# Kernel optimization log

Hardware: AMD Instinct MI355X
Metric: run time of the kernel (lower is better)

## Reference

```python
import jax, jax.numpy as jnp
import numpy as np

N_USER = 100000
N_ITEM = 50000
D = 64
NNZ_A = 2000000
NNZ_S = 1000000
N_TAIL = 10000
N_HEAD = 4000
K = 10
B = 4096
N_NEG = 4
CONV = 40.0
ILAYERS = 3
SLAYERS = 2


def setup_inputs() -> dict:
    key = jax.random.key(0)
    ks = jax.random.split(key, 18)
    return {
        'user_emb': 0.1 * jax.random.normal(ks[0], (N_USER, D), jnp.float32),
        'item_emb': 0.1 * jax.random.normal(ks[1], (N_ITEM, D), jnp.float32),
        'w0': 0.05 * jax.random.normal(ks[2], (256, D), jnp.float32),
        'b0': 0.05 * jax.random.normal(ks[3], (256,), jnp.float32),
        'w2': 0.05 * jax.random.normal(ks[4], (D, 256), jnp.float32),
        'b2': 0.05 * jax.random.normal(ks[5], (D,), jnp.float32),
        'a_vals': jax.random.uniform(ks[6], (NNZ_A,), jnp.float32) * 0.1,
        's_vals': jax.random.uniform(ks[7], (NNZ_S,), jnp.float32) * 0.1,
        'item_degree': jax.random.uniform(ks[8], (N_ITEM,), jnp.float32) * 100.0,
        'a_rows': jax.random.randint(ks[9], (NNZ_A,), 0, N_USER + N_ITEM, jnp.int32),
        'a_cols': jax.random.randint(ks[10], (NNZ_A,), 0, N_USER + N_ITEM, jnp.int32),
        's_rows': jax.random.randint(ks[11], (NNZ_S,), 0, N_USER, jnp.int32),
        's_cols': jax.random.randint(ks[12], (NNZ_S,), 0, N_USER, jnp.int32),
        'tail_idx': jax.random.randint(ks[13], (N_TAIL,), 0, N_ITEM, jnp.int32),
        'head_idx': jax.random.randint(ks[14], (N_HEAD,), 0, N_ITEM, jnp.int32),
        'batch_user': jax.random.randint(ks[15], (B,), 0, N_USER, jnp.int32),
        'batch_pos': jax.random.randint(ks[16], (B,), 0, N_ITEM, jnp.int32),
        'batch_neg': jax.random.randint(ks[17], (B, N_NEG), 0, N_ITEM, jnp.int32),
    }


def _spmm(vals, rows, cols, x, n):
    # sparse.mm(A, x) with A in COO form; duplicate indices sum (coalesce/CSR semantics)
    return jax.ops.segment_sum(vals[:, None] * x[cols], rows, num_segments=n)


def reference(user_emb, item_emb, w0, b0, w2, b2, a_vals, s_vals, item_degree,
              a_rows, a_cols, s_rows, s_cols, tail_idx, head_idx,
              batch_user, batch_pos, batch_neg):
    # ---- item_link_predict_v1 (training branch: plain linear, no ReLU) ----
    def enc(f):
        return (f @ w0.T + b0) @ w2.T + b2
    tail_e = enc(item_emb[tail_idx])          # [N_TAIL, D]
    top_e = enc(item_emb[head_idx])           # [N_HEAD, D]
    scores = tail_e @ top_e.T                 # [N_TAIL, N_HEAD]
    topv, topi = jax.lax.top_k(scores, K)     # [N_TAIL, K]
    s = jax.nn.sigmoid(topv)
    w = s / (jnp.sum(s, axis=1, keepdims=True) + 1.0)
    ig_rows = jnp.repeat(tail_idx, K)         # tail index repeated per topk
    ig_cols = head_idx[topi].reshape(-1)
    ig_vals = jax.lax.stop_gradient(w.reshape(-1))  # original detaches enhance_weight
    # ---- interaction-graph propagation (LightGCN-style, last layer kept) ----
    n_total = N_USER + N_ITEM
    all_emb = jnp.concatenate([user_emb, item_emb], axis=0)
    for _ in range(ILAYERS):
        all_emb = _spmm(a_vals, a_rows, a_cols, all_emb, n_total)
    users = all_emb[:N_USER]
    items = all_emb[N_USER:]
    # ---- social-graph propagation, mean over layer outputs ----
    u_acc = users
    u = users
    for _ in range(SLAYERS):
        u = _spmm(s_vals, s_rows, s_cols, u, N_USER)
        u_acc = u_acc + u
    users_final = u_acc / float(SLAYERS + 1)
    # ---- item-similarity-graph enhancement with degree-based reweighting ----
    item_enh = _spmm(ig_vals, ig_rows, ig_cols, items, N_ITEM)
    sum_weight = CONV / (CONV + jnp.exp(item_degree / CONV))  # [N_ITEM]
    items_final = items + sum_weight[:, None] * item_enh
    # ---- BPR-style softplus loss + L2 reg on initial embeddings ----
    ue = users_final[batch_user]              # [B, D]
    pe = items_final[batch_pos]               # [B, D]
    ne = items_final[batch_neg]               # [B, N_NEG, D]
    pos_scores = jnp.sum(ue * pe, axis=1)
    neg_scores = jnp.mean(jnp.sum(ue[:, None, :] * ne, axis=2), axis=1)
    loss = jnp.mean(jax.nn.softplus(neg_scores - pos_scores))
    u0 = user_emb[batch_user]
    p0 = item_emb[batch_pos]
    n0 = item_emb[batch_neg]
    reg = 0.5 * (jnp.sum(u0 ** 2) + jnp.sum(p0 ** 2) + jnp.sum(n0 ** 2)) / float(B)
    return (loss, reg)
```

## Files before the change

### kernel.cpp

```cpp
#include <hip/hip_runtime.h>
#include <hip/hip_bf16.h>
#include <hip/hip_fp8.h>

#define N_USERC 100000
#define N_ITEMC 50000
#define N_TOTALC 150000
#define DC 64
#define NNZ_AC 2000000
#define NNZ_SC 1000000
#define N_TAILC 10000
#define N_HEADC 4000
#define TOPKC 10
#define BATCHC 4096
#define N_NEGC 4
#define CONVF 40.0f
#define CHUNK_ROWS 5000

#define RPB 256
#define NB_A ((N_TOTALC + RPB - 1) / RPB)
#define NB_S ((N_USERC + RPB - 1) / RPB)
#define IPB 6144
#define PBLK_A ((NNZ_AC + IPB - 1) / IPB)
#define PBLK_S ((NNZ_SC + IPB - 1) / IPB)
#define SLAB 4096
#define FCAP 4096

#define LOSS_BLOCKS (BATCHC / 4)

__device__ __forceinline__ unsigned char F2Q(float f) {
    __hip_fp8_e4m3 q(f);
    return (unsigned char)q.__x;
}
__device__ __forceinline__ float Q2F(unsigned char b) {
    __hip_fp8_e4m3 q;
    q.__x = (__hip_fp8_storage_t)b;
    return (float)q;
}
__device__ __forceinline__ unsigned short F2H(float f) {
    __hip_bfloat16 b = __float2bfloat16(f);
    return *(unsigned short*)&b;
}

__global__ __launch_bounds__(256) void init_cursors(int* __restrict__ aCur, int* __restrict__ sCur) {
    int i = blockIdx.x * 256 + threadIdx.x;
    if (i < NB_A) aCur[i] = i * SLAB;
    if (i < NB_S) sCur[i] = i * SLAB;
}

__global__ __launch_bounds__(256) void partition_fused(
    const float* __restrict__ a_vals, const int* __restrict__ a_rows, const int* __restrict__ a_cols,
    const float* __restrict__ s_vals, const int* __restrict__ s_rows, const int* __restrict__ s_cols,
    int* __restrict__ aCur, int* __restrict__ sCur,
    int2* __restrict__ aPack, int2* __restrict__ sPack) {
    __shared__ int h[NB_A];
    __shared__ int cur[NB_A];
    int blk = blockIdx.x;
    const float* vals; const int* rows; const int* cols; int n; int nb; int* gcur; int2* pack; int base;
    if (blk < PBLK_A) { vals = a_vals; rows = a_rows; cols = a_cols; n = NNZ_AC; nb = NB_A; gcur = aCur; pack = aPack; base = blk * IPB; }
    else { vals = s_vals; rows = s_rows; cols = s_cols; n = NNZ_SC; nb = NB_S; gcur = sCur; pack = sPack; base = (blk - PBLK_A) * IPB; }
    int tid = threadIdx.x;
    for (int i = tid; i < nb; i += 256) h[i] = 0;
    __syncthreads();
    for (int k = 0; k < IPB; k += 256) {
        int idx = base + k + tid;
        if (idx < n) atomicAdd(&h[rows[idx] >> 8], 1);
    }
    __syncthreads();
    for (int i = tid; i < nb; i += 256) {
        int c = h[i];
        cur[i] = c ? atomicAdd(&gcur[i], c) : 0;
    }
    __syncthreads();
    for (int k = 0; k < IPB; k += 256) {
        int idx = base + k + tid;
        if (idx < n) {
            int r = rows[idx];
            int b = r >> 8;
            int pos = atomicAdd(&cur[b], 1);
            pack[pos] = make_int2(__float_as_int(vals[idx]), cols[idx] | ((r & 255) << 18));
        }
    }
}

__global__ __launch_bounds__(256) void csr_finalize(const int* __restrict__ aEnd, const int* __restrict__ sEnd,
                                                    const int2* __restrict__ aRaw, const int2* __restrict__ sRaw,
                                                    int2* __restrict__ aOut, int2* __restrict__ sOut,
                                                    int* __restrict__ aRs, int* __restrict__ aRe,
                                                    int* __restrict__ sRs, int* __restrict__ sRe) {
    __shared__ int2 ebuf[FCAP];
    __shared__ int cnt_[RPB];
    __shared__ int scn[RPB];
    __shared__ int cursor[RPB];
    int blk = blockIdx.x;
    const int* ends; const int2* raw; int2* outp; int* rs; int* re; int nrows; int b;
    if (blk < NB_A) { ends = aEnd; raw = aRaw; outp = aOut; rs = aRs; re = aRe; nrows = N_TOTALC; b = blk; }
    else { ends = sEnd; raw = sRaw; outp = sOut; rs = sRs; re = sRe; nrows = N_USERC; b = blk - NB_A; }
    int s = b * SLAB;
    int e = ends[b];
    int n = e - s;
    int tid = threadIdx.x;
    bool useLds = (n <= FCAP);
    cnt_[tid] = 0;
    __syncthreads();
    if (useLds) {
        for (int i = tid; i < n; i += 256) {
            int2 en = raw[s + i];
            ebuf[i] = en;
            atomicAdd(&cnt_[(en.y >> 18) & 255], 1);
        }
    } else {
        for (int i = tid; i < n; i += 256)
            atomicAdd(&cnt_[(raw[s + i].y >> 18) & 255], 1);
    }
    __syncthreads();
    scn[tid] = cnt_[tid];
    __syncthreads();
    for (int off = 1; off < RPB; off <<= 1) {
        int t = (tid >= off) ? scn[tid - off] : 0;
        __syncthreads();
        scn[tid] += t;
        __syncthreads();
    }
    {
        int inc = scn[tid];
        int ex = inc - cnt_[tid];
        cursor[tid] = ex;
        int row = (b << 8) + tid;
        if (row < nrows) { rs[row] = s + ex; re[row] = s + inc; }
    }
    __syncthreads();
    if (useLds) {
        for (int i = tid; i < n; i += 256) {
            int2 en = ebuf[i];
            int r = (en.y >> 18) & 255;
            int pos = atomicAdd(&cursor[r], 1);
            outp[s + pos] = make_int2(en.x, en.y & 0x3FFFF);
        }
    } else {
        for (int i = tid; i < n; i += 256) {
            int2 en = raw[s + i];
            int r = (en.y >> 18) & 255;
            int pos = atomicAdd(&cursor[r], 1);
            outp[s + pos] = make_int2(en.x, en.y & 0x3FFFF);
        }
    }
}

__global__ __launch_bounds__(256) void to_f8_concat(const float* __restrict__ xu, const float* __restrict__ xi,
                                                    unsigned char* __restrict__ out) {
    size_t i4 = (size_t)blockIdx.x * 256 + threadIdx.x;
    const size_t NU4 = (size_t)N_USERC * 16;
    const size_t NT4 = (size_t)N_TOTALC * 16;
    if (i4 >= NT4) return;
    float4 v = (i4 < NU4) ? ((const float4*)xu)[i4] : ((const float4*)xi)[i4 - NU4];
    uchar4 q;
    q.x = F2Q(v.x); q.y = F2Q(v.y); q.z = F2Q(v.z); q.w = F2Q(v.w);
    ((uchar4*)out)[i4] = q;
}

__global__ __launch_bounds__(256) void spmm_f8(const int* __restrict__ rps, const int* __restrict__ rpe,
                                               const int2* __restrict__ pack,
                                               const unsigned char* __restrict__ xq,
                                               float* __restrict__ y,
                                               unsigned char* __restrict__ yq, int nrows) {
    int w = (blockIdx.x * blockDim.x + threadIdx.x) >> 6;
    int lane = threadIdx.x & 63;
    if (w >= nrows) return;
    int half = lane >> 5;
    int sl = lane & 31;
    int s = rps[w], e = rpe[w];
    float a0 = 0.f, a1 = 0.f, b0 = 0.f, b1 = 0.f;
    float c0 = 0.f, c1 = 0.f, d0 = 0.f, d1 = 0.f;
    if (e > s) {
        int last = e - 1;
        for (int j = s; j < e; j += 16) {
            int k0 = j + half, k1 = k0 + 2, k2 = k0 + 4, k3 = k0 + 6;
            int k4 = k0 + 8, k5 = k0 + 10, k6 = k0 + 12, k7 = k0 + 14;
            int2 e0 = pack[min(k0, last)], e1 = pack[min(k1, last)];
            int2 e2 = pack[min(k2, last)], e3 = pack[min(k3, last)];
            int2 e4 = pack[min(k4, last)], e5 = pack[min(k5, last)];
            int2 e6 = pack[min(k6, last)], e7 = pack[min(k7, last)];
            unsigned short g0 = *(const unsigned short*)&xq[(size_t)e0.y * 64 + sl * 2];
            unsigned short g1 = *(const unsigned short*)&xq[(size_t)e1.y * 64 + sl * 2];
            unsigned short g2 = *(const unsigned short*)&xq[(size_t)e2.y * 64 + sl * 2];
            unsigned short g3 = *(const unsigned short*)&xq[(size_t)e3.y * 64 + sl * 2];
            unsigned short g4 = *(const unsigned short*)&xq[(size_t)e4.y * 64 + sl * 2];
            unsigned short g5 = *(const unsigned short*)&xq[(size_t)e5.y * 64 + sl * 2];
            unsigned short g6 = *(const unsigned short*)&xq[(size_t)e6.y * 64 + sl * 2];
            unsigned short g7 = *(const unsigned short*)&xq[(size_t)e7.y * 64 + sl * 2];
            float v0 = (k0 <= last) ? __int_as_float(e0.x) : 0.f;
            float v1 = (k1 <= last) ? __int_as_float(e1.x) : 0.f;
            float v2 = (k2 <= last) ? __int_as_float(e2.x) : 0.f;
            float v3 = (k3 <= last) ? __int_as_float(e3.x) : 0.f;
            float v4 = (k4 <= last) ? __int_as_float(e4.x) : 0.f;
            float v5 = (k5 <= last) ? __int_as_float(e5.x) : 0.f;
            float v6 = (k6 <= last) ? __int_as_float(e6.x) : 0.f;
            float v7 = (k7 <= last) ? __int_as_float(e7.x) : 0.f;
            a0 += v0 * Q2F((unsigned char)(g0 & 255)); a1 += v0 * Q2F((unsigned char)(g0 >> 8));
            b0 += v1 * Q2F((unsigned char)(g1 & 255)); b1 += v1 * Q2F((unsigned char)(g1 >> 8));
            c0 += v2 * Q2F((unsigned char)(g2 & 255)); c1 += v2 * Q2F((unsigned char)(g2 >> 8));
            d0 += v3 * Q2F((unsigned char)(g3 & 255)); d1 += v3 * Q2F((unsigned char)(g3 >> 8));
            a0 += v4 * Q2F((unsigned char)(g4 & 255)); a1 += v4 * Q2F((unsigned char)(g4 >> 8));
            b0 += v5 * Q2F((unsigned char)(g5 & 255)); b1 += v5 * Q2F((unsigned char)(g5 >> 8));
            c0 += v6 * Q2F((unsigned char)(g6 & 255)); c1 += v6 * Q2F((unsigned char)(g6 >> 8));
            d0 += v7 * Q2F((unsigned char)(g7 & 255)); d1 += v7 * Q2F((unsigned char)(g7 >> 8));
        }
    }
    float r0 = (a0 + b0) + (c0 + d0);
    float r1 = (a1 + b1) + (c1 + d1);
    r0 += __shfl_xor(r0, 32, 64);
    r1 += __shfl_xor(r1, 32, 64);
    if (lane < 32) {
        if (y) ((float2*)y)[(size_t)w * 32 + sl] = make_float2(r0, r1);
        if (yq) { uchar2 q; q.x = F2Q(r0); q.y = F2Q(r1); ((uchar2*)yq)[(size_t)w * 32 + sl] = q; }
    }
}

__global__ __launch_bounds__(256) void mc_kernel(const float* __restrict__ w0, const float* __restrict__ b0,
                                                 const float* __restrict__ w2, const float* __restrict__ b2,
                                                 float* __restrict__ Mrm, float* __restrict__ cvec) {
    int idx = blockIdx.x * 256 + threadIdx.x;
    if (idx < 4096) {
        int j = idx >> 6, d = idx & 63;
        float acc = 0.f;
        for (int k = 0; k < 256; ++k) acc += w2[j * 256 + k] * w0[k * 64 + d];
        Mrm[idx] = acc;
    } else if (idx < 4160) {
        int i = idx - 4096;
        float acc = b2[i];
        for (int k = 0; k < 256; ++k) acc += w2[i * 256 + k] * b0[k];
        cvec[i] = acc;
    }
}

__global__ __launch_bounds__(256) void enc2_fused(const float* __restrict__ emb,
                                                  const int* __restrict__ tail_idx, const int* __restrict__ head_idx,
                                                  const float* __restrict__ Mrm, const float* __restrict__ cvec,
                                                  float* __restrict__ tail_e, float* __restrict__ top_e) {
    __shared__ float fsh[4][64];
    int wv = threadIdx.x >> 6, lane = threadIdx.x & 63;
    int r = blockIdx.x * 4 + wv;
    int item;
    float* outp;
    if (r < N_TAILC) { item = tail_idx[r]; outp = tail_e + (size_t)r * 64; }
    else if (r < N_TAILC + N_HEADC) { item = head_idx[r - N_TAILC]; outp = top_e + (size_t)(r - N_TAILC) * 64; }
    else { item = -1; outp = nullptr; }
    if (item >= 0) fsh[wv][lane] = emb[(size_t)item * 64 + lane];
    __syncthreads();
    if (item < 0) return;
    float acc = cvec[lane];
#pragma unroll
    for (int d4 = 0; d4 < 64; d4 += 4) {
        float4 m4 = *(const float4*)&Mrm[lane * 64 + d4];
        float4 f4 = *(const float4*)&fsh[wv][d4];
        acc += m4.x * f4.x + m4.y * f4.y + m4.z * f4.z + m4.w * f4.w;
    }
    outp[lane] = acc;
}

__global__ __launch_bounds__(256) void score_gemm(const float* __restrict__ A,
                                                  const float* __restrict__ B,
                                                  unsigned short* __restrict__ C, int M) {
    __shared__ float As[32][132];
    __shared__ float Bs[32][132];
    int tid = threadIdx.x;
    int tx = tid & 15, ty = tid >> 4;
    int rowbase = blockIdx.y * 128;
    int colbase = blockIdx.x * 128;
    float acc[8][8];
#pragma unroll
    for (int i = 0; i < 8; ++i)
#pragma unroll
        for (int j = 0; j < 8; ++j) acc[i][j] = 0.f;

    for (int k0 = 0; k0 < 64; k0 += 32) {
        __syncthreads();
#pragma unroll
        for (int i = 0; i < 4; ++i) {
            int f = tid + i * 256;
            int r = f >> 3;
            int kq = (f & 7) << 2;
            int grow = rowbase + r;
            float4 av = (grow < M) ? *(const float4*)&A[(size_t)grow * 64 + k0 + kq]
                                   : make_float4(0.f, 0.f, 0.f, 0.f);
            As[kq + 0][r] = av.x; As[kq + 1][r] = av.y; As[kq + 2][r] = av.z; As[kq + 3][r] = av.w;
            int gcol = colbase + r;
            float4 bv = (gcol < N_HEADC) ? *(const float4*)&B[(size_t)gcol * 64 + k0 + kq]
                                         : make_float4(0.f, 0.f, 0.f, 0.f);
            Bs[kq + 0][r] = bv.x; Bs[kq + 1][r] = bv.y; Bs[kq + 2][r] = bv.z; Bs[kq + 3][r] = bv.w;
        }
        __syncthreads();
#pragma unroll
        for (int k = 0; k < 32; ++k) {
            float a[8], b[8];
#pragma unroll
            for (int i = 0; i < 8; ++i) a[i] = As[k][ty + 16 * i];
#pragma unroll
            for (int j = 0; j < 8; ++j) b[j] = Bs[k][tx + 16 * j];
#pragma unroll
            for (int i = 0; i < 8; ++i)
#pragma unroll
                for (int j = 0; j < 8; ++j) acc[i][j] += a[i] * b[j];
        }
    }
#pragma unroll
    for (int i = 0; i < 8; ++i) {
        int r = rowbase + ty + 16 * i;
        if (r < M) {
#pragma unroll
            for (int j = 0; j < 8; ++j) {
                int c = colbase + tx + 16 * j;
                if (c < N_HEADC) C[(size_t)r * N_HEADC + c] = F2H(acc[i][j]);
            }
        }
    }
}

#define BUB(vk, ik) { if (cv > vk) { float tf = vk; vk = cv; cv = tf; int ti = ik; ik = ci; ci = ti; } }
#define TINS(sc, idx) { float sc_ = (sc); if (sc_ > v9) { float cv = sc_; int ci = (idx); \
    BUB(v0, i0) BUB(v1, i1) BUB(v2, i2) BUB(v3, i3) BUB(v4, i4) \
    BUB(v5, i5) BUB(v6, i6) BUB(v7, i7) BUB(v8, i8) BUB(v9, i9) } }
#define BLO(u) __uint_as_float((u) << 16)
#define BHI(u) __uint_as_float((u) & 0xFFFF0000u)

__global__ __launch_bounds__(256) void topk_rows(const unsigned short* __restrict__ scores, int nrows, int row0,
                                                 const int* __restrict__ head_idx,
                                                 int* __restrict__ ig_cols, float* __restrict__ ig_vals) {
    int w = (blockIdx.x * blockDim.x + threadIdx.x) >> 6;
    int lane = threadIdx.x & 63;
    if (w >= nrows) return;
    const unsigned short* srow = scores + (size_t)w * N_HEADC;
    float v0 = -1e30f, v1 = -1e30f, v2 = -1e30f, v3 = -1e30f, v4 = -1e30f;
    float v5 = -1e30f, v6 = -1e30f, v7 = -1e30f, v8 = -1e30f, v9 = -1e30f;
    int i0 = -1, i1 = -1, i2 = -1, i3 = -1, i4 = -1;
    int i5 = -1, i6 = -1, i7 = -1, i8 = -1, i9 = -1;
    for (int it = 0; it < 8; ++it) {
        int f8 = lane + it * 64;
        if (f8 < 500) {
            uint4 s8 = ((const uint4*)srow)[f8];
            int cb = f8 * 8;
            TINS(BLO(s8.x), cb + 0)
            TINS(BHI(s8.x), cb + 1)
            TINS(BLO(s8.y), cb + 2)
            TINS(BHI(s8.y), cb + 3)
            TINS(BLO(s8.z), cb + 4)
            TINS(BHI(s8.z), cb + 5)
            TINS(BLO(s8.w), cb + 6)
            TINS(BHI(s8.w), cb + 7)
        }
    }
    float ssum = 0.f;
    float outv = 0.f;
    int outid = -1;
#pragma unroll
    for (int r = 0; r < TOPKC; ++r) {
        float cv = v0;
        int ci = i0;
        int wl = lane;
#pragma unroll
        for (int m = 1; m < 64; m <<= 1) {
            float ov = __shfl_xor(cv, m, 64);
            int oi = __shfl_xor(ci, m, 64);
            int ol = __shfl_xor(wl, m, 64);
            if (ov > cv || (ov == cv && ol < wl)) { cv = ov; ci = oi; wl = ol; }
        }
        if (wl == lane) {
            v0 = v1; i0 = i1; v1 = v2; i1 = i2; v2 = v3; i2 = i3;
            v3 = v4; i3 = i4; v4 = v5; i4 = i5; v5 = v6; i5 = i6;
            v6 = v7; i6 = i7; v7 = v8; i7 = i8; v8 = v9; i8 = i9;
            v9 = -1e30f; i9 = -1;
        }
        ssum += 1.f / (1.f + expf(-cv));
        if (lane == r) { outv = cv; outid = ci; }
    }
    if (lane < TOPKC) {
        float s = 1.f / (1.f + expf(-outv));
        float wgt = s / (ssum + 1.f);
        int grow = row0 + w;
        ig_vals[grow * TOPKC + lane] = wgt;
        ig_cols[grow * TOPKC + lane] = head_idx[outid];
    }
}

__global__ __launch_bounds__(256) void ig_spmm_kernel(const int* __restrict__ tail_idx,
                                                      const int* __restrict__ ig_cols,
                                                      const float* __restrict__ ig_vals,
                                                      const float* __restrict__ items,
                                                      float* __restrict__ enh) {
    int r = (blockIdx.x * blockDim.x + threadIdx.x) >> 6;
    int lane = threadIdx.x & 63;
    if (r >= N_TAILC) return;
    int row = tail_idx[r];
    float acc = 0.f;
#pragma unroll
    for (int k = 0; k < TOPKC; ++k) {
        int col = ig_cols[r * TOPKC + k];
        float wgt = ig_vals[r * TOPKC + k];
        acc += wgt * items[(size_t)col * 64 + lane];
    }
    atomicAdd(&enh[(size_t)row * 64 + lane], acc);
}

__global__ __launch_bounds__(256) void loss_kernel(const float* __restrict__ u0, const float* __restrict__ u1,
                                                   const float* __restrict__ u2, const float* __restrict__ items,
                                                   const float* __restrict__ enh, const float* __restrict__ deg,
                                                   const float* __restrict__ user_emb, const float* __restrict__ item_emb,
                                                   const int* __restrict__ bu, const int* __restrict__ bp,
                                                   const int* __restrict__ bn, float* __restrict__ part) {
    __shared__ float lsum[4], rsum[4];
    int w = (blockIdx.x * blockDim.x + threadIdx.x) >> 6;
    int wv = threadIdx.x >> 6;
    int lane = threadIdx.x & 63;
    int uu = bu[w], pp = bp[w];
    float ue = (u0[uu * 64 + lane] + u1[uu * 64 + lane] + u2[uu * 64 + lane]) * (1.f / 3.f);
    float swp = CONVF / (CONVF + expf(deg[pp] * (1.f / CONVF)));
    float pe = items[pp * 64 + lane] + swp * enh[pp * 64 + lane];
    float ps = ue * pe;
    float ns = 0.f;
    float u0e = user_emb[uu * 64 + lane];
    float p0e = item_emb[pp * 64 + lane];
    float reg = u0e * u0e + p0e * p0e;
#pragma unroll
    for (int k = 0; k < N_NEGC; ++k) {
        int nn = bn[w * N_NEGC + k];
        float swn = CONVF / (CONVF + expf(deg[nn] * (1.f / CONVF)));
        float nv = items[nn * 64 + lane] + swn * enh[nn * 64 + lane];
        ns += ue * nv;
        float n0 = item_emb[nn * 64 + lane];
        reg += n0 * n0;
    }
#pragma unroll
    for (int m = 32; m >= 1; m >>= 1) {
        ps += __shfl_xor(ps, m, 64);
        ns += __shfl_xor(ns, m, 64);
        reg += __shfl_xor(reg, m, 64);
    }
    if (lane == 0) {
        float x = ns * (1.f / N_NEGC) - ps;
        float sp = (x > 0.f) ? (x + log1pf(expf(-x))) : log1pf(expf(x));
        lsum[wv] = sp;
        rsum[wv] = reg;
    }
    __syncthreads();
    if (threadIdx.x == 0) {
        part[blockIdx.x] = lsum[0] + lsum[1] + lsum[2] + lsum[3];
        part[LOSS_BLOCKS + blockIdx.x] = rsum[0] + rsum[1] + rsum[2] + rsum[3];
    }
}

__global__ __launch_bounds__(256) void loss_reduce(const float* __restrict__ part, float* __restrict__ out) {
    __shared__ float l[256], r[256];
    int tid = threadIdx.x;
    float a = 0.f, b = 0.f;
    for (int i = tid; i < LOSS_BLOCKS; i += 256) {
        a += part[i];
        b += part[LOSS_BLOCKS + i];
    }
    l[tid] = a; r[tid] = b;
    __syncthreads();
    for (int off = 128; off >= 1; off >>= 1) {
        if (tid < off) { l[tid] += l[tid + off]; r[tid] += r[tid + off]; }
        __syncthreads();
    }
    if (tid == 0) {
        out[0] = l[0] * (1.f / BATCHC);
        out[1] = 0.5f * r[0] * (1.f / BATCHC);
    }
}

extern "C" void kernel_launch(void* const* d_in, const int* in_sizes, int n_in,
                              void* d_out, int out_size, void* d_ws, size_t ws_size,
                              hipStream_t stream) {
    const float* user_emb = (const float*)d_in[0];
    const float* item_emb = (const float*)d_in[1];
    const float* w0 = (const float*)d_in[2];
    const float* b0 = (const float*)d_in[3];
    const float* w2 = (const float*)d_in[4];
    const float* b2 = (const float*)d_in[5];
    const float* a_vals = (const float*)d_in[6];
    const float* s_vals = (const float*)d_in[7];
    const float* item_degree = (const float*)d_in[8];
    const int* a_rows = (const int*)d_in[9];
    const int* a_cols = (const int*)d_in[10];
    const int* s_rows = (const int*)d_in[11];
    const int* s_cols = (const int*)d_in[12];
    const int* tail_idx = (const int*)d_in[13];
    const int* head_idx = (const int*)d_in[14];
    const int* batch_user = (const int*)d_in[15];
    const int* batch_pos = (const int*)d_in[16];
    const int* batch_neg = (const int*)d_in[17];
    float* out = (float*)d_out;

    char* p = (char*)d_ws;
    auto carve = [&](size_t bytes) -> void* {
        void* r = (void*)p;
        p += (bytes + 255) & ~size_t(255);
        return r;
    };
    float* embB = (float*)carve((size_t)N_TOTALC * 64 * 4);
    float* u1 = (float*)carve((size_t)N_USERC * 64 * 4);
    float* u2 = (float*)carve((size_t)N_USERC * 64 * 4);
    float* enh = (float*)carve((size_t)N_ITEMC * 64 * 4);
    float* tail_e = (float*)carve((size_t)N_TAILC * 64 * 4);
    float* top_e = (float*)carve((size_t)N_HEADC * 64 * 4);
    int2* aSort = (int2*)carve((size_t)NB_A * SLAB * 8);
    int2* sSort = (int2*)carve((size_t)NB_S * SLAB * 8);
    int* aRs = (int*)carve((size_t)N_TOTALC * 4);
    int* aRe = (int*)carve((size_t)N_TOTALC * 4);
    int* sRs = (int*)carve((size_t)N_USERC * 4);
    int* sRe = (int*)carve((size_t)N_USERC * 4);
    int* aCur = (int*)carve((size_t)NB_A * 4);
    int* sCur = (int*)carve((size_t)NB_S * 4);
    int* ig_cols_buf = (int*)carve((size_t)N_TAILC * TOPKC * 4);
    float* ig_vals_buf = (float*)carve((size_t)N_TAILC * TOPKC * 4);
    float* Mrm = (float*)carve(64 * 64 * 4);
    float* cvec = (float*)carve(64 * 4);
    float* loss_part = (float*)carve((size_t)LOSS_BLOCKS * 2 * 4);
    char* scratch = (char*)carve((size_t)40 * 1024 * 1024);
    int2* aPackRaw = (int2*)scratch;
    int2* sPackRaw = aPackRaw + (size_t)NB_A * SLAB;
    unsigned short* scores = (unsigned short*)scratch;
    unsigned char* f0 = (unsigned char*)scratch;
    unsigned char* f1 = f0 + (size_t)N_TOTALC * 64;
    unsigned char* f2 = f1 + (size_t)N_TOTALC * 64;
    unsigned char* f3 = f2 + (size_t)N_TOTALC * 64;
    unsigned char* uF1 = f0;

    init_cursors<<<(NB_A + 255) / 256, 256, 0, stream>>>(aCur, sCur);
    partition_fused<<<PBLK_A + PBLK_S, 256, 0, stream>>>(a_vals, a_rows, a_cols,
                                                         s_vals, s_rows, s_cols,
                                                         aCur, sCur, aPackRaw, sPackRaw);
    csr_finalize<<<NB_A + NB_S, 256, 0, stream>>>(aCur, sCur, aPackRaw, sPackRaw,
                                                  aSort, sSort, aRs, aRe, sRs, sRe);

    mc_kernel<<<17, 256, 0, stream>>>(w0, b0, w2, b2, Mrm, cvec);
    enc2_fused<<<(N_TAILC + N_HEADC + 3) / 4, 256, 0, stream>>>(item_emb, tail_idx, head_idx, Mrm, cvec, tail_e, top_e);

    for (int row0 = 0; row0 < N_TAILC; row0 += CHUNK_ROWS) {
        int m = N_TAILC - row0;
        if (m > CHUNK_ROWS) m = CHUNK_ROWS;
        int rb = (m + 127) / 128;
        score_gemm<<<dim3((N_HEADC + 127) / 128, rb), 256, 0, stream>>>(tail_e + (size_t)row0 * 64, top_e, scores, m);
        topk_rows<<<(m + 3) / 4, 256, 0, stream>>>(scores, m, row0, head_idx, ig_cols_buf, ig_vals_buf);
    }

    to_f8_concat<<<((N_TOTALC * 16) + 255) / 256, 256, 0, stream>>>(user_emb, item_emb, f0);

    {
        int blocks = (N_TOTALC + 3) / 4;
        spmm_f8<<<blocks, 256, 0, stream>>>(aRs, aRe, aSort, f0, nullptr, f1, N_TOTALC);
        spmm_f8<<<blocks, 256, 0, stream>>>(aRs, aRe, aSort, f1, nullptr, f2, N_TOTALC);
        spmm_f8<<<blocks, 256, 0, stream>>>(aRs, aRe, aSort, f2, embB, f3, N_TOTALC);
    }
    const float* u0 = embB;
    const float* items = embB + (size_t)N_USERC * 64;

    {
        int blocks = (N_USERC + 3) / 4;
        spmm_f8<<<blocks, 256, 0, stream>>>(sRs, sRe, sSort, f3, u1, uF1, N_USERC);
        spmm_f8<<<blocks, 256, 0, stream>>>(sRs, sRe, sSort, uF1, u2, nullptr, N_USERC);
    }

    hipMemsetAsync(enh, 0, (size_t)N_ITEMC * 64 * 4, stream);
    ig_spmm_kernel<<<(N_TAILC + 3) / 4, 256, 0, stream>>>(tail_idx, ig_cols_buf, ig_vals_buf, items, enh);

    loss_kernel<<<LOSS_BLOCKS, 256, 0, stream>>>(u0, u1, u2, items, enh, item_degree,
                                                 user_emb, item_emb, batch_user, batch_pos, batch_neg, loss_part);
    loss_reduce<<<1, 256, 0, stream>>>(loss_part, out);
}
```

Before: 651.8 us.

## Compute tail-head score GEMM with bf16 MFMA instead of FP32 SIMT tiles

The encoder now writes tail and head embeddings as bf16. The tiled FP32 shared-memory score GEMM is replaced by a per-wave bf16 MFMA kernel that computes a 16x32 output tile from direct global loads. This is meant to cut the compute cost of the 10000x4000x64 score matrix and halve the embedding storage it reads. The trade-offs are lower input precision, which could flip top-k choices on near ties, and uncoalesced 2-byte scattered stores with no shared-memory reuse of the operands.

```diff
diff --git a/kernel.cpp b/kernel.cpp
--- a/kernel.cpp
+++ b/kernel.cpp
@@ -24,8 +24,13 @@
 #define PBLK_S ((NNZ_SC + IPB - 1) / IPB)
 #define SLAB 4096
 #define FCAP 4096
+#define NCG 125
+#define RT_CHUNK ((CHUNK_ROWS + 15) / 16)
 
 #define LOSS_BLOCKS (BATCHC / 4)
+
+typedef __attribute__((ext_vector_type(8))) short short8v;
+typedef __attribute__((ext_vector_type(4))) float f32x4;
 
 __device__ __forceinline__ unsigned char F2Q(float f) {
     __hip_fp8_e4m3 q(f);
@@ -236,12 +241,12 @@
 __global__ __launch_bounds__(256) void enc2_fused(const float* __restrict__ emb,
                                                   const int* __restrict__ tail_idx, const int* __restrict__ head_idx,
                                                   const float* __restrict__ Mrm, const float* __restrict__ cvec,
-                                                  float* __restrict__ tail_e, float* __restrict__ top_e) {
+                                                  unsigned short* __restrict__ tail_e, unsigned short* __restrict__ top_e) {
     __shared__ float fsh[4][64];
     int wv = threadIdx.x >> 6, lane = threadIdx.x & 63;
     int r = blockIdx.x * 4 + wv;
     int item;
-    float* outp;
+    unsigned short* outp;
     if (r < N_TAILC) { item = tail_idx[r]; outp = tail_e + (size_t)r * 64; }
     else if (r < N_TAILC + N_HEADC) { item = head_idx[r - N_TAILC]; outp = top_e + (size_t)(r - N_TAILC) * 64; }
     else { item = -1; outp = nullptr; }
@@ -255,63 +260,40 @@
         float4 f4 = *(const float4*)&fsh[wv][d4];
         acc += m4.x * f4.x + m4.y * f4.y + m4.z * f4.z + m4.w * f4.w;
     }
-    outp[lane] = acc;
-}
-
-__global__ __launch_bounds__(256) void score_gemm(const float* __restrict__ A,
-                                                  const float* __restrict__ B,
-                                                  unsigned short* __restrict__ C, int M) {
-    __shared__ float As[32][132];
-    __shared__ float Bs[32][132];
-    int tid = threadIdx.x;
-    int tx = tid & 15, ty = tid >> 4;
-    int rowbase = blockIdx.y * 128;
-    int colbase = blockIdx.x * 128;
-    float acc[8][8];
-#pragma unroll
-    for (int i = 0; i < 8; ++i)
-#pragma unroll
-        for (int j = 0; j < 8; ++j) acc[i][j] = 0.f;
-
-    for (int k0 = 0; k0 < 64; k0 += 32) {
-        __syncthreads();
-#pragma unroll
-        for (int i = 0; i < 4; ++i) {
-            int f = tid + i * 256;
-            int r = f >> 3;
-            int kq = (f & 7) << 2;
-            int grow = rowbase + r;
-            float4 av = (grow < M) ? *(const float4*)&A[(size_t)grow * 64 + k0 + kq]
-                                   : make_float4(0.f, 0.f, 0.f, 0.f);
-            As[kq + 0][r] = av.x; As[kq + 1][r] = av.y; As[kq + 2][r] = av.z; As[kq + 3][r] = av.w;
-            int gcol = colbase + r;
-            float4 bv = (gcol < N_HEADC) ? *(const float4*)&B[(size_t)gcol * 64 + k0 + kq]
-                                         : make_float4(0.f, 0.f, 0.f, 0.f);
-            Bs[kq + 0][r] = bv.x; Bs[kq + 1][r] = bv.y; Bs[kq + 2][r] = bv.z; Bs[kq + 3][r] = bv.w;
-        }
-        __syncthreads();
-#pragma unroll
-        for (int k = 0; k < 32; ++k) {
-            float a[8], b[8];
-#pragma unroll
-            for (int i = 0; i < 8; ++i) a[i] = As[k][ty + 16 * i];
-#pragma unroll
-            for (int j = 0; j < 8; ++j) b[j] = Bs[k][tx + 16 * j];
-#pragma unroll
-            for (int i = 0; i < 8; ++i)
-#pragma unroll
-                for (int j = 0; j < 8; ++j) acc[i][j] += a[i] * b[j];
-        }
-    }
-#pragma unroll
-    for (int i = 0; i < 8; ++i) {
-        int r = rowbase + ty + 16 * i;
-        if (r < M) {
-#pragma unroll
-            for (int j = 0; j < 8; ++j) {
-                int c = colbase + tx + 16 * j;
-                if (c < N_HEADC) C[(size_t)r * N_HEADC + c] = F2H(acc[i][j]);
-            }
+    outp[lane] = F2H(acc);
+}
+
+__global__ __launch_bounds__(256) void score_gemm_mfma(const unsigned short* __restrict__ AH,
+                                                       const unsigned short* __restrict__ BH,
+                                                       unsigned short* __restrict__ C, int M) {
+    int gw = (blockIdx.x * 256 + threadIdx.x) >> 6;
+    int lane = threadIdx.x & 63;
+    int RT = (M + 15) >> 4;
+    if (gw >= RT * NCG) return;
+    int rt = gw / NCG, cg = gw % NCG;
+    int rowbase = rt << 4, colbase = cg << 5;
+    int r = lane & 15, kg = lane >> 4;
+    int arow = rowbase + r; if (arow >= M) arow = M - 1;
+    const short8v a0 = *(const short8v*)(AH + (size_t)arow * 64 + kg * 8);
+    const short8v a1 = *(const short8v*)(AH + (size_t)arow * 64 + 32 + kg * 8);
+    const unsigned short* b0p = BH + (size_t)(colbase + r) * 64 + kg * 8;
+    const unsigned short* b1p = BH + (size_t)(colbase + 16 + r) * 64 + kg * 8;
+    const short8v b00 = *(const short8v*)(b0p);
+    const short8v b01 = *(const short8v*)(b0p + 32);
+    const short8v b10 = *(const short8v*)(b1p);
+    const short8v b11 = *(const short8v*)(b1p + 32);
+    f32x4 acc0 = {0.f, 0.f, 0.f, 0.f};
+    f32x4 acc1 = {0.f, 0.f, 0.f, 0.f};
+    acc0 = __builtin_amdgcn_mfma_f32_16x16x32_bf16(a0, b00, acc0, 0, 0, 0);
+    acc0 = __builtin_amdgcn_mfma_f32_16x16x32_bf16(a1, b01, acc0, 0, 0, 0);
+    acc1 = __builtin_amdgcn_mfma_f32_16x16x32_bf16(a0, b10, acc1, 0, 0, 0);
+    acc1 = __builtin_amdgcn_mfma_f32_16x16x32_bf16(a1, b11, acc1, 0, 0, 0);
+#pragma unroll
+    for (int q = 0; q < 4; ++q) {
+        int row = rowbase + (kg << 2) + q;
+        if (row < M) {
+            C[(size_t)row * N_HEADC + colbase + r] = F2H(acc0[q]);
+            C[(size_t)row * N_HEADC + colbase + 16 + r] = F2H(acc1[q]);
         }
     }
 }
@@ -501,8 +483,8 @@
     float* u1 = (float*)carve((size_t)N_USERC * 64 * 4);
     float* u2 = (float*)carve((size_t)N_USERC * 64 * 4);
     float* enh = (float*)carve((size_t)N_ITEMC * 64 * 4);
-    float* tail_e = (float*)carve((size_t)N_TAILC * 64 * 4);
-    float* top_e = (float*)carve((size_t)N_HEADC * 64 * 4);
+    unsigned short* tail_e = (unsigned short*)carve((size_t)N_TAILC * 64 * 2);
+    unsigned short* top_e = (unsigned short*)carve((size_t)N_HEADC * 64 * 2);
     int2* aSort = (int2*)carve((size_t)NB_A * SLAB * 8);
     int2* sSort = (int2*)carve((size_t)NB_S * SLAB * 8);
     int* aRs = (int*)carve((size_t)N_TOTALC * 4);
@@ -539,8 +521,8 @@
     for (int row0 = 0; row0 < N_TAILC; row0 += CHUNK_ROWS) {
         int m = N_TAILC - row0;
         if (m > CHUNK_ROWS) m = CHUNK_ROWS;
-        int rb = (m + 127) / 128;
-        score_gemm<<<dim3((N_HEADC + 127) / 128, rb), 256, 0, stream>>>(tail_e + (size_t)row0 * 64, top_e, scores, m);
+        int waves = ((m + 15) / 16) * NCG;
+        score_gemm_mfma<<<(waves + 3) / 4, 256, 0, stream>>>(tail_e + (size_t)row0 * 64, top_e, scores, m);
         topk_rows<<<(m + 3) / 4, 256, 0, stream>>>(scores, m, row0, head_idx, ig_cols_buf, ig_vals_buf);
     }
 
```

Result: faster. 547.7 us (-16.0%).
